# Performance work log

Hardware: AMD Instinct MI355X
Metric: run time of the kernel (lower is better)

## Reference

```python
import jax, jax.numpy as jnp
import numpy as np

T, D, H = 1024, 256, 256


def mish(x):
    return x * jnp.tanh(jax.nn.softplus(x))


def layer_norm(x, w, b, eps=1e-5):
    mu = x.mean(-1, keepdims=True)
    var = ((x - mu) ** 2).mean(-1, keepdims=True)
    return (x - mu) / jnp.sqrt(var + eps) * w + b


def setup_inputs() -> dict:
    key = jax.random.key(0)
    ks = jax.random.split(key, 12)
    def glorot(k, sh, fan_in):
        return (jax.random.normal(k, sh, jnp.float32) / np.sqrt(fan_in)).astype(jnp.float32)
    return {
        "x": jax.random.normal(ks[0], (T, D), jnp.float32),
        "s0": jnp.zeros((1, H, H), jnp.float32),
        "z0": jnp.zeros((1, H), jnp.float32),
        "start": jax.random.randint(ks[1], (T + 1,), 0, 2, jnp.int32),
        "done": jax.random.randint(ks[2], (T + 1,), 0, 2, jnp.int32),
        "Wk": glorot(ks[3], (H, D), D),
        "Wq": glorot(ks[4], (H, D), D),
        "Wv": glorot(ks[5], (H, D), D),
        "Wskip": glorot(ks[6], (H, D), D),
        "bskip": jnp.zeros((H,), jnp.float32),
        "W1": glorot(ks[7], (H, H), H),
        "b1": jnp.zeros((H,), jnp.float32),
        "W2": glorot(ks[8], (H, H), H),
        "b2": jnp.zeros((H,), jnp.float32),
        "W3": glorot(ks[9], (H, H), H),
        "b3": jnp.zeros((H,), jnp.float32),
        "ln_w": jnp.ones((H,), jnp.float32),
        "ln_b": jnp.zeros((H,), jnp.float32),
    }


def reference(x, s0, z0, start, done, Wk, Wq, Wv, Wskip, bskip, W1, b1, W2, b2, W3, b3, ln_w, ln_b):
    # feature maps (equinox Linear: y = W @ x, weight is (out,in))
    k = jax.nn.elu(x @ Wk.T)          # [T,H]
    q = jax.nn.elu(x @ Wq.T)          # [T,H]
    v = x @ Wv.T                      # [T,H]
    st = start.astype(x.dtype)[:, None]   # [T+1,1] reset-continuation flags
    dn = done.astype(x.dtype)[:, None]    # [T+1,1]
    # prepend carried state to the sequence, as in the original
    kv = jnp.concatenate([s0, jnp.einsum('ti,tj->tij', k, v)], axis=0)  # [T+1,H,H]
    kk = jnp.concatenate([z0, k], axis=0)                               # [T+1,H]
    def combine(a, b):
        s_a, z_a, _, _ = a
        kv_b, k_b, st_b, dn_b = b
        s = s_a * st_b[..., None] + kv_b * dn_b[..., None]
        z = z_a * st_b + k_b * dn_b
        return (s, z, st_b, dn_b)
    s, z, _, _ = jax.lax.associative_scan(combine, (kv, kk, st, dn))
    # drop the initial-state slot so time indices align with queries
    s_t, z_t = s[1:], z[1:]                          # [T,H,H], [T,H]
    numer = jnp.einsum('ti,tij->tj', q, s_t)         # [T,H]
    denom = jnp.einsum('ti,tj->t', z_t, q).clip(1e-5)  # faithful to source einsum
    out = numer / denom[:, None]
    h = mish(out @ W1.T + b1)
    h = mish(h @ W2.T + b2)
    h = h @ W3.T + b3
    return layer_norm(h + (x @ Wskip.T + bskip), ln_w, ln_b)
```

## Files before the change

### kernel.cpp

```cpp
#include <hip/hip_runtime.h>
#include <math.h>


typedef unsigned long long u64;
typedef unsigned short u16;
typedef __attribute__((ext_vector_type(8))) unsigned short us8;
typedef __attribute__((ext_vector_type(4))) unsigned short us4;
typedef __attribute__((ext_vector_type(8))) short s8;
typedef __attribute__((ext_vector_type(4))) float f4;

__device__ __forceinline__ float eluf(float v) { return v > 0.f ? v : expm1f(v); }
__device__ __forceinline__ float mishf(float v) {
  float sp = fmaxf(v, 0.f) + log1pf(expf(-fabsf(v)));
  return v * tanhf(sp);
}
__device__ __forceinline__ u16 f2bf(float f) {
  unsigned u = __float_as_uint(f);
  unsigned r = u + 0x7FFFu + ((u >> 16) & 1u);
  return (u16)(r >> 16);
}
__device__ __forceinline__ float bf2f(u16 h) { return __uint_as_float((unsigned)h << 16); }

__device__ __forceinline__ f4 mfma16(const u16* a, const u16* b, f4 c) {
  s8 av = *(const s8*)(const void*)a;
  s8 bv = *(const s8*)(const void*)b;
  return __builtin_amdgcn_mfma_f32_16x16x32_bf16(av, bv, c, 0, 0, 0);
}

__device__ __forceinline__ u64 expand32(u64 x) {
  x &= 0xFFFFFFFFull;
  x = (x | (x << 16)) & 0x0000FFFF0000FFFFull;
  x = (x | (x << 8))  & 0x00FF00FF00FF00FFull;
  x = (x | (x << 4))  & 0x0F0F0F0F0F0F0F0Full;
  x = (x | (x << 2))  & 0x3333333333333333ull;
  x = (x | (x << 1))  & 0x5555555555555555ull;
  return x | (x << 1);
}

__device__ __forceinline__ us8 cvt8v(float4 a, float4 b) {
  us8 v;
  v[0] = f2bf(a.x); v[1] = f2bf(a.y); v[2] = f2bf(a.z); v[3] = f2bf(a.w);
  v[4] = f2bf(b.x); v[5] = f2bf(b.y); v[6] = f2bf(b.z); v[7] = f2bf(b.w);
  return v;
}

__global__ __launch_bounds__(256) void qkvs_mfma(const float* __restrict__ x,
    const float* __restrict__ Wk, const float* __restrict__ Wq,
    const float* __restrict__ Wv, const float* __restrict__ Wsk,
    const float* __restrict__ bskip,
    const float* __restrict__ W1, const float* __restrict__ W2, const float* __restrict__ W3,
    u16* __restrict__ Kb, u16* __restrict__ Qb, u16* __restrict__ Vb,
    float* __restrict__ SKP, float* __restrict__ Kpart, u16* __restrict__ Wb) {
  __shared__ u16 Xs[64 * 40], Ws[64 * 40];
  const int tid = threadIdx.x, wave = tid >> 6, l = tid & 63;
  const int l15 = l & 15, quad = l >> 4;
  const int rt = blockIdx.x & 15, my = blockIdx.x >> 4;
  const int mat = my >> 2, nt = my & 3;
  const int n0 = nt * 64, mbase = rt * 64;
  const float* Wsrc = (mat == 0) ? Wk : (mat == 1) ? Wq : (mat == 2) ? Wv : Wsk;
  if (tid < 192) {
    int cidx = blockIdx.x * 768 + tid * 4;
    const float* Wm = (cidx < 65536) ? W1 : (cidx < 131072) ? W2 : W3;
    float4 v = *(const float4*)(Wm + (cidx & 65535));
    us4 o; o.x = f2bf(v.x); o.y = f2bf(v.y); o.z = f2bf(v.z); o.w = f2bf(v.w);
    *(us4*)&Wb[cidx] = o;
  }
  f4 acc[4];
#pragma unroll
  for (int s = 0; s < 4; s++) acc[s] = (f4){0.f, 0.f, 0.f, 0.f};
  const int srow = tid >> 2, sko = (tid & 3) * 8;
  const float* xp = &x[(mbase + srow) * 256 + sko];
  const float* wp = &Wsrc[(n0 + srow) * 256 + sko];
  float4 xa = *(const float4*)xp, xb = *(const float4*)(xp + 4);
  float4 wa = *(const float4*)wp, wc = *(const float4*)(wp + 4);
#pragma unroll 1
  for (int kt = 0; kt < 8; kt++) {
    *(us8*)&Xs[srow * 40 + sko] = cvt8v(xa, xb);
    *(us8*)&Ws[srow * 40 + sko] = cvt8v(wa, wc);
    if (kt < 7) {
      xa = *(const float4*)(xp + (kt + 1) * 32);
      xb = *(const float4*)(xp + (kt + 1) * 32 + 4);
      wa = *(const float4*)(wp + (kt + 1) * 32);
      wc = *(const float4*)(wp + (kt + 1) * 32 + 4);
    }
    __syncthreads();
    const u16* ap = &Xs[(wave * 16 + l15) * 40 + quad * 8];
#pragma unroll
    for (int s = 0; s < 4; s++)
      acc[s] = mfma16(ap, &Ws[(s * 16 + l15) * 40 + quad * 8], acc[s]);
    __syncthreads();
  }
  const int mw = mbase + wave * 16 + quad * 4;
  if (mat == 0) {
    float tmp[4][4];
#pragma unroll
    for (int s = 0; s < 4; s++)
#pragma unroll
      for (int r = 0; r < 4; r++) {
        float v = eluf(acc[s][r]);
        tmp[s][r] = v;
        Kb[(mw + r) * 256 + n0 + s * 16 + l15] = f2bf(v);
      }
#pragma unroll
    for (int r = 0; r < 4; r++) {
      float t = tmp[0][r] + tmp[1][r] + tmp[2][r] + tmp[3][r];
#pragma unroll
      for (int off = 1; off <= 8; off <<= 1) t += __shfl_xor(t, off);
      if (l15 == 0) Kpart[nt * 1024 + mw + r] = t;
    }
  } else if (mat == 1) {
#pragma unroll
    for (int s = 0; s < 4; s++)
#pragma unroll
      for (int r = 0; r < 4; r++)
        Qb[(mw + r) * 256 + n0 + s * 16 + l15] = f2bf(eluf(acc[s][r]));
  } else if (mat == 2) {
#pragma unroll
    for (int s = 0; s < 4; s++)
#pragma unroll
      for (int r = 0; r < 4; r++)
        Vb[(mw + r) * 256 + n0 + s * 16 + l15] = f2bf(acc[s][r]);
  } else {
#pragma unroll
    for (int s = 0; s < 4; s++) {
      int n = n0 + s * 16 + l15;
      float bv = bskip[n];
#pragma unroll
      for (int r = 0; r < 4; r++)
        SKP[(mw + r) * 256 + n] = acc[s][r] + bv;
    }
  }
}

__global__ __launch_bounds__(512) void attn_mlp(
    const u16* __restrict__ Kb, const u16* __restrict__ Qb, const u16* __restrict__ Vb,
    const float* __restrict__ Kpart, const float* __restrict__ SKP,
    const int* __restrict__ start, const int* __restrict__ done,
    const u16* __restrict__ Wb,
    const float* __restrict__ b1, const float* __restrict__ b2, const float* __restrict__ b3,
    const float* __restrict__ lnw, const float* __restrict__ lnb,
    float* __restrict__ outp) {
  __shared__ u64 GS[37];
  __shared__ u64 Mw[64];
  __shared__ u16 As[16 * 264];
  __shared__ float Op[8][256];
  __shared__ float dp[8];
  __shared__ float Hbuf[4 * 260];
  const int tid = threadIdx.x, wave = tid >> 6, l = tid & 63;
  const int l15 = l & 15, quad = l >> 4;
  const int m0 = blockIdx.x * 4;
  for (int job = wave; job < 37; job += 8) {
    int lv, w;
    if (job < 17)      { lv = 0; w = job; }
    else if (job < 25) { lv = 1; w = job - 17; }
    else if (job < 29) { lv = 2; w = job - 25; }
    else if (job < 31) { lv = 3; w = job - 29; }
    else               { lv = job - 27; w = 0; }
    int n = 1024 >> lv;
    int j = w * 64 + l;
    int ok = 0;
    if (j < n)
      ok = (j & 1) ? (done[((j + 1) << lv) - 1] != 0) : (start[((j + 2) << lv) - 1] != 0);
    u64 word = __ballot(ok != 0);
    if (l == 0) GS[(lv == 0) ? w : (lv == 1) ? 17 + w : (lv == 2) ? 25 + w
                   : (lv == 3) ? 29 + w : 27 + lv] = word;
  }
  __syncthreads();
  const int GOFF2[10] = {0, 17, 25, 29, 31, 32, 33, 34, 35, 36};
  if (wave < 4) {
    const int t = m0 + wave + 1;
    int rr10 = t;
#pragma unroll
    for (int q = 0; q < 10; q++) rr10 = (rr10 & 1) ? (rr10 >> 1) : (rr10 >> 1) - 1;
    u64 cur = (l == 0 && rr10 == 0) ? 1ull : 0ull;
#pragma unroll 1
    for (int lv = 9; lv >= 1; lv--) {
      int rr = t;
      for (int q = 0; q < lv; q++) rr = (rr & 1) ? (rr >> 1) : (rr >> 1) - 1;
      const int nw = (lv >= 4) ? 1 : (8 >> (lv - 1));
      u64 pw = __shfl(cur, l >> 1);
      u64 word;
      if (rr <= 0) word = (l == 0 && rr == 0) ? 1ull : 0ull;
      else {
        u64 e = 0;
        if (l < nw) e = expand32((l & 1) ? (pw >> 32) : pw) & GS[GOFF2[lv] + l];
        if (rr & 1) word = e;
        else {
          int gi = ((rr + 1) << lv) - 1;
          word = (start[gi] != 0) ? e : 0ull;
          if ((rr >> 6) == l) word |= (u64)(done[gi] != 0) << (rr & 63);
        }
        if (l >= nw) word = 0ull;
      }
      cur = word;
    }
    u64 pw = __shfl(cur, (l >> 1) & 7);
    u64 uw = 0;
    if (l <= 16) {
      u64 e = 0;
      if (l < 16) e = expand32((l & 1) ? (pw >> 32) : pw) & GS[l];
      if (t & 1) uw = e;
      else {
        uw = (start[t] != 0) ? e : 0ull;
        if ((t >> 6) == l) uw |= (u64)(done[t] != 0) << (t & 63);
      }
    }
    u64 nxt = __shfl(uw, (l + 1) & 63);
    u64 mw0 = (uw >> 1) | (nxt << 63);
    if (l < 16) Mw[wave * 16 + l] = mw0;
  }
  __syncthreads();
  const int r = wave & 3, h = wave >> 2;
  const int tp = m0 + r;
  float q[4], O[4] = {0.f, 0.f, 0.f, 0.f};
  {
    us4 qv = *(const us4*)&Qb[tp * 256 + l * 4];
    q[0] = bf2f(qv.x); q[1] = bf2f(qv.y); q[2] = bf2f(qv.z); q[3] = bf2f(qv.w);
  }
  float qs = q[0] + q[1] + q[2] + q[3];
#pragma unroll
  for (int off = 1; off <= 32; off <<= 1) qs += __shfl_xor(qs, off);
  float d = 0.f;
  for (int w = h * 8; w < h * 8 + 8; w++) {
    u64 bits = Mw[r * 16 + w];
    while (bits) {
      int b0 = __builtin_ctzll(bits); bits &= bits - 1;
      int j0 = w * 64 + b0;
      if (bits) {
        int b1x = __builtin_ctzll(bits); bits &= bits - 1;
        int j1 = w * 64 + b1x;
        us4 k0 = *(const us4*)&Kb[j0 * 256 + l * 4];
        us4 v0 = *(const us4*)&Vb[j0 * 256 + l * 4];
        us4 k1 = *(const us4*)&Kb[j1 * 256 + l * 4];
        us4 v1 = *(const us4*)&Vb[j1 * 256 + l * 4];
        float s0 = q[0] * bf2f(k0.x) + q[1] * bf2f(k0.y) + q[2] * bf2f(k0.z) + q[3] * bf2f(k0.w);
        float s1 = q[0] * bf2f(k1.x) + q[1] * bf2f(k1.y) + q[2] * bf2f(k1.z) + q[3] * bf2f(k1.w);
#pragma unroll
        for (int off = 1; off <= 32; off <<= 1) {
          s0 += __shfl_xor(s0, off);
          s1 += __shfl_xor(s1, off);
        }
        d += (Kpart[j0] + Kpart[1024 + j0] + Kpart[2048 + j0] + Kpart[3072 + j0]) +
             (Kpart[j1] + Kpart[1024 + j1] + Kpart[2048 + j1] + Kpart[3072 + j1]);
        O[0] += s0 * bf2f(v0.x) + s1 * bf2f(v1.x);
        O[1] += s0 * bf2f(v0.y) + s1 * bf2f(v1.y);
        O[2] += s0 * bf2f(v0.z) + s1 * bf2f(v1.z);
        O[3] += s0 * bf2f(v0.w) + s1 * bf2f(v1.w);
      } else {
        us4 k0 = *(const us4*)&Kb[j0 * 256 + l * 4];
        us4 v0 = *(const us4*)&Vb[j0 * 256 + l * 4];
        float s0 = q[0] * bf2f(k0.x) + q[1] * bf2f(k0.y) + q[2] * bf2f(k0.z) + q[3] * bf2f(k0.w);
#pragma unroll
        for (int off = 1; off <= 32; off <<= 1) s0 += __shfl_xor(s0, off);
        d += Kpart[j0] + Kpart[1024 + j0] + Kpart[2048 + j0] + Kpart[3072 + j0];
        O[0] += s0 * bf2f(v0.x); O[1] += s0 * bf2f(v0.y);
        O[2] += s0 * bf2f(v0.z); O[3] += s0 * bf2f(v0.w);
      }
    }
  }
#pragma unroll
  for (int i = 0; i < 4; i++) Op[wave][l * 4 + i] = O[i];
  if (l == 0) dp[wave] = d;
  __syncthreads();
  if (h == 0) {
    float dd = dp[r] + dp[r + 4];
    float inv = 1.f / fmaxf(qs * dd, 1e-5f);
    us4 o;
    o.x = f2bf((O[0] + Op[r + 4][l * 4 + 0]) * inv);
    o.y = f2bf((O[1] + Op[r + 4][l * 4 + 1]) * inv);
    o.z = f2bf((O[2] + Op[r + 4][l * 4 + 2]) * inv);
    o.w = f2bf((O[3] + Op[r + 4][l * 4 + 3]) * inv);
    *(us4*)&As[r * 264 + l * 4] = o;
  }
  __syncthreads();
#pragma unroll 1
  for (int layer = 0; layer < 3; layer++) {
    const u16* Wl = Wb + layer * 65536;
    const float* bias = (layer == 0) ? b1 : (layer == 1) ? b2 : b3;
    f4 acc[2];
#pragma unroll
    for (int c = 0; c < 2; c++) {
      const int nt = wave * 2 + c;
      acc[c] = (f4){0.f, 0.f, 0.f, 0.f};
#pragma unroll
      for (int kt = 0; kt < 8; kt++) {
        us8 bf = *(const us8*)&Wl[(nt * 16 + l15) * 256 + kt * 32 + quad * 8];
        acc[c] = mfma16(&As[l15 * 264 + kt * 32 + quad * 8], (const u16*)&bf, acc[c]);
      }
    }
    __syncthreads();
    if (quad == 0) {
#pragma unroll
      for (int c = 0; c < 2; c++) {
        const int n = (wave * 2 + c) * 16 + l15;
        float bv = bias[n];
        if (layer < 2) {
#pragma unroll
          for (int rr = 0; rr < 4; rr++)
            As[rr * 264 + n] = f2bf(mishf(acc[c][rr] + bv));
        } else {
#pragma unroll
          for (int rr = 0; rr < 4; rr++)
            Hbuf[rr * 260 + n] = acc[c][rr] + bv + SKP[(m0 + rr) * 256 + n];
        }
      }
    }
    __syncthreads();
  }
  if (wave < 4) {
    float hv[4];
#pragma unroll
    for (int i = 0; i < 4; i++) hv[i] = Hbuf[wave * 260 + l * 4 + i];
    float s1 = hv[0] + hv[1] + hv[2] + hv[3];
    float s2 = hv[0] * hv[0] + hv[1] * hv[1] + hv[2] * hv[2] + hv[3] * hv[3];
#pragma unroll
    for (int off = 1; off <= 32; off <<= 1) {
      s1 += __shfl_xor(s1, off);
      s2 += __shfl_xor(s2, off);
    }
    float mu = s1 * (1.f / 256.f);
    float var = s2 * (1.f / 256.f) - mu * mu;
    float rs = rsqrtf(fmaxf(var, 0.f) + 1e-5f);
    float4 wv = *(const float4*)&lnw[l * 4];
    float4 bv = *(const float4*)&lnb[l * 4];
    float4 o;
    o.x = (hv[0] - mu) * rs * wv.x + bv.x;
    o.y = (hv[1] - mu) * rs * wv.y + bv.y;
    o.z = (hv[2] - mu) * rs * wv.z + bv.z;
    o.w = (hv[3] - mu) * rs * wv.w + bv.w;
    *(float4*)&outp[(m0 + wave) * 256 + l * 4] = o;
  }
}

extern "C" void kernel_launch(void* const* d_in, const int* in_sizes, int n_in,
                              void* d_out, int out_size, void* d_ws, size_t ws_size,
                              hipStream_t stream) {
  (void)in_sizes; (void)n_in; (void)out_size; (void)ws_size;
  const float* x   = (const float*)d_in[0];
  const int* start = (const int*)d_in[3];
  const int* done  = (const int*)d_in[4];
  const float* Wk  = (const float*)d_in[5];
  const float* Wq  = (const float*)d_in[6];
  const float* Wv  = (const float*)d_in[7];
  const float* Wsk = (const float*)d_in[8];
  const float* bsk = (const float*)d_in[9];
  const float* W1  = (const float*)d_in[10];
  const float* b1  = (const float*)d_in[11];
  const float* W2  = (const float*)d_in[12];
  const float* b2  = (const float*)d_in[13];
  const float* W3  = (const float*)d_in[14];
  const float* b3  = (const float*)d_in[15];
  const float* lnw = (const float*)d_in[16];
  const float* lnb = (const float*)d_in[17];
  float* out = (float*)d_out;

  char* w = (char*)d_ws;
  u16* Kb      = (u16*)w;
  u16* Qb      = (u16*)(w + 524288);
  u16* Vb      = (u16*)(w + 1048576);
  float* SKP   = (float*)(w + 1572864);
  float* Kpart = (float*)(w + 2621440);
  u16* Wb      = (u16*)(w + 2637824);

  qkvs_mfma<<<256, 256, 0, stream>>>(x, Wk, Wq, Wv, Wsk, bsk, W1, W2, W3,
                                     Kb, Qb, Vb, SKP, Kpart, Wb);
  attn_mlp<<<256, 512, 0, stream>>>(Kb, Qb, Vb, Kpart, SKP, start, done, Wb,
                                    b1, b2, b3, lnw, lnb, out);
}
```

Measured before the change: 129.5 us.

## Fuse projection and attention kernels into one cooperative launch with grid sync

Merges the QKV/skip projection kernel and the attention+MLP kernel into a single cooperative kernel separated by a grid-wide barrier. The projection GEMM now reads fp32 operands directly into registers and drops the LDS staging and block barriers, with each of 8 waves computing two 16x16 tiles. The start/done mask ballots and scan-mask computation run before the grid sync so they overlap the projection work. This aims to remove one kernel launch gap and shared-memory round trips, at the cost of a grid-wide sync and the occupancy requirement that all 256 blocks be co-resident.

```diff
diff --git a/kernel.cpp b/kernel.cpp
--- a/kernel.cpp
+++ b/kernel.cpp
@@ -1,6 +1,9 @@
 #include <hip/hip_runtime.h>
+#include <hip/hip_cooperative_groups.h>
 #include <math.h>
 
+
+namespace cg = cooperative_groups;
 
 typedef unsigned long long u64;
 typedef unsigned short u16;
@@ -44,126 +47,122 @@
   return v;
 }
 
-__global__ __launch_bounds__(256) void qkvs_mfma(const float* __restrict__ x,
-    const float* __restrict__ Wk, const float* __restrict__ Wq,
-    const float* __restrict__ Wv, const float* __restrict__ Wsk,
-    const float* __restrict__ bskip,
-    const float* __restrict__ W1, const float* __restrict__ W2, const float* __restrict__ W3,
+__global__ __launch_bounds__(512) void fused(
+    const float* __restrict__ x, const float* __restrict__ Wk,
+    const float* __restrict__ Wq, const float* __restrict__ Wv,
+    const float* __restrict__ Wsk, const float* __restrict__ bskip,
+    const int* __restrict__ start, const int* __restrict__ done,
+    const float* __restrict__ W1, const float* __restrict__ W2,
+    const float* __restrict__ W3, const float* __restrict__ b1,
+    const float* __restrict__ b2, const float* __restrict__ b3,
+    const float* __restrict__ lnw, const float* __restrict__ lnb,
     u16* __restrict__ Kb, u16* __restrict__ Qb, u16* __restrict__ Vb,
-    float* __restrict__ SKP, float* __restrict__ Kpart, u16* __restrict__ Wb) {
-  __shared__ u16 Xs[64 * 40], Ws[64 * 40];
-  const int tid = threadIdx.x, wave = tid >> 6, l = tid & 63;
-  const int l15 = l & 15, quad = l >> 4;
-  const int rt = blockIdx.x & 15, my = blockIdx.x >> 4;
-  const int mat = my >> 2, nt = my & 3;
-  const int n0 = nt * 64, mbase = rt * 64;
-  const float* Wsrc = (mat == 0) ? Wk : (mat == 1) ? Wq : (mat == 2) ? Wv : Wsk;
-  if (tid < 192) {
-    int cidx = blockIdx.x * 768 + tid * 4;
-    const float* Wm = (cidx < 65536) ? W1 : (cidx < 131072) ? W2 : W3;
-    float4 v = *(const float4*)(Wm + (cidx & 65535));
-    us4 o; o.x = f2bf(v.x); o.y = f2bf(v.y); o.z = f2bf(v.z); o.w = f2bf(v.w);
-    *(us4*)&Wb[cidx] = o;
-  }
-  f4 acc[4];
-#pragma unroll
-  for (int s = 0; s < 4; s++) acc[s] = (f4){0.f, 0.f, 0.f, 0.f};
-  const int srow = tid >> 2, sko = (tid & 3) * 8;
-  const float* xp = &x[(mbase + srow) * 256 + sko];
-  const float* wp = &Wsrc[(n0 + srow) * 256 + sko];
-  float4 xa = *(const float4*)xp, xb = *(const float4*)(xp + 4);
-  float4 wa = *(const float4*)wp, wc = *(const float4*)(wp + 4);
-#pragma unroll 1
-  for (int kt = 0; kt < 8; kt++) {
-    *(us8*)&Xs[srow * 40 + sko] = cvt8v(xa, xb);
-    *(us8*)&Ws[srow * 40 + sko] = cvt8v(wa, wc);
-    if (kt < 7) {
-      xa = *(const float4*)(xp + (kt + 1) * 32);
-      xb = *(const float4*)(xp + (kt + 1) * 32 + 4);
-      wa = *(const float4*)(wp + (kt + 1) * 32);
-      wc = *(const float4*)(wp + (kt + 1) * 32 + 4);
-    }
-    __syncthreads();
-    const u16* ap = &Xs[(wave * 16 + l15) * 40 + quad * 8];
-#pragma unroll
-    for (int s = 0; s < 4; s++)
-      acc[s] = mfma16(ap, &Ws[(s * 16 + l15) * 40 + quad * 8], acc[s]);
-    __syncthreads();
-  }
-  const int mw = mbase + wave * 16 + quad * 4;
-  if (mat == 0) {
-    float tmp[4][4];
-#pragma unroll
-    for (int s = 0; s < 4; s++)
-#pragma unroll
-      for (int r = 0; r < 4; r++) {
-        float v = eluf(acc[s][r]);
-        tmp[s][r] = v;
-        Kb[(mw + r) * 256 + n0 + s * 16 + l15] = f2bf(v);
-      }
-#pragma unroll
-    for (int r = 0; r < 4; r++) {
-      float t = tmp[0][r] + tmp[1][r] + tmp[2][r] + tmp[3][r];
-#pragma unroll
-      for (int off = 1; off <= 8; off <<= 1) t += __shfl_xor(t, off);
-      if (l15 == 0) Kpart[nt * 1024 + mw + r] = t;
-    }
-  } else if (mat == 1) {
-#pragma unroll
-    for (int s = 0; s < 4; s++)
-#pragma unroll
-      for (int r = 0; r < 4; r++)
-        Qb[(mw + r) * 256 + n0 + s * 16 + l15] = f2bf(eluf(acc[s][r]));
-  } else if (mat == 2) {
-#pragma unroll
-    for (int s = 0; s < 4; s++)
-#pragma unroll
-      for (int r = 0; r < 4; r++)
-        Vb[(mw + r) * 256 + n0 + s * 16 + l15] = f2bf(acc[s][r]);
-  } else {
-#pragma unroll
-    for (int s = 0; s < 4; s++) {
-      int n = n0 + s * 16 + l15;
-      float bv = bskip[n];
-#pragma unroll
-      for (int r = 0; r < 4; r++)
-        SKP[(mw + r) * 256 + n] = acc[s][r] + bv;
-    }
-  }
-}
-
-__global__ __launch_bounds__(512) void attn_mlp(
-    const u16* __restrict__ Kb, const u16* __restrict__ Qb, const u16* __restrict__ Vb,
-    const float* __restrict__ Kpart, const float* __restrict__ SKP,
-    const int* __restrict__ start, const int* __restrict__ done,
-    const u16* __restrict__ Wb,
-    const float* __restrict__ b1, const float* __restrict__ b2, const float* __restrict__ b3,
-    const float* __restrict__ lnw, const float* __restrict__ lnb,
+    float* __restrict__ SKP, float* __restrict__ Kpart, u16* __restrict__ Wb,
     float* __restrict__ outp) {
   __shared__ u64 GS[37];
   __shared__ u64 Mw[64];
+  __shared__ float scrK[128];
   __shared__ u16 As[16 * 264];
   __shared__ float Op[8][256];
   __shared__ float dp[8];
   __shared__ float Hbuf[4 * 260];
   const int tid = threadIdx.x, wave = tid >> 6, l = tid & 63;
   const int l15 = l & 15, quad = l >> 4;
-  const int m0 = blockIdx.x * 4;
-  for (int job = wave; job < 37; job += 8) {
-    int lv, w;
-    if (job < 17)      { lv = 0; w = job; }
-    else if (job < 25) { lv = 1; w = job - 17; }
-    else if (job < 29) { lv = 2; w = job - 25; }
-    else if (job < 31) { lv = 3; w = job - 29; }
-    else               { lv = job - 27; w = 0; }
-    int n = 1024 >> lv;
-    int j = w * 64 + l;
-    int ok = 0;
-    if (j < n)
-      ok = (j & 1) ? (done[((j + 1) << lv) - 1] != 0) : (start[((j + 2) << lv) - 1] != 0);
-    u64 word = __ballot(ok != 0);
-    if (l == 0) GS[(lv == 0) ? w : (lv == 1) ? 17 + w : (lv == 2) ? 25 + w
-                   : (lv == 3) ? 29 + w : 27 + lv] = word;
+  const int b = blockIdx.x;
+  const int m0 = b * 4;
+
+  if (tid < 192) {
+    int cidx = b * 768 + tid * 4;
+    const float* Wm = (cidx < 65536) ? W1 : (cidx < 131072) ? W2 : W3;
+    float4 v = *(const float4*)(Wm + (cidx & 65535));
+    us4 o; o.x = f2bf(v.x); o.y = f2bf(v.y); o.z = f2bf(v.z); o.w = f2bf(v.w);
+    *(us4*)&Wb[cidx] = o;
+  }
+
+  const int rt = b & 15, my = b >> 4, mat = my >> 2, nt = my & 3;
+  const int n0 = nt * 64, mbase = rt * 64;
+  const float* Wsrc = (mat == 0) ? Wk : (mat == 1) ? Wq : (mat == 2) ? Wv : Wsk;
+  const int st = wave & 3, sh = (wave >> 2) * 2;
+  const int arow = mbase + st * 16 + l15;
+  f4 acc[2];
+  acc[0] = (f4){0.f, 0.f, 0.f, 0.f};
+  acc[1] = (f4){0.f, 0.f, 0.f, 0.f};
+  {
+    const float* apb = x + (size_t)arow * 256 + quad * 8;
+    const float* bp0 = Wsrc + (size_t)(n0 + sh * 16 + l15) * 256 + quad * 8;
+    const float* bp1 = bp0 + 16 * 256;
+#pragma unroll 1
+    for (int kt = 0; kt < 8; kt++) {
+      const int ko = kt * 32;
+      float4 a0 = *(const float4*)(apb + ko), a1 = *(const float4*)(apb + ko + 4);
+      float4 c0 = *(const float4*)(bp0 + ko), c1 = *(const float4*)(bp0 + ko + 4);
+      float4 d0 = *(const float4*)(bp1 + ko), d1 = *(const float4*)(bp1 + ko + 4);
+      us8 af = cvt8v(a0, a1);
+      us8 bf0 = cvt8v(c0, c1);
+      us8 bf1 = cvt8v(d0, d1);
+      acc[0] = mfma16((const u16*)&af, (const u16*)&bf0, acc[0]);
+      acc[1] = mfma16((const u16*)&af, (const u16*)&bf1, acc[1]);
+    }
+  }
+  const int mw = mbase + st * 16 + quad * 4;
+  if (mat == 0) {
+    float tw[4];
+#pragma unroll
+    for (int r = 0; r < 4; r++) {
+      float v0 = eluf(acc[0][r]), v1 = eluf(acc[1][r]);
+      Kb[(mw + r) * 256 + n0 + sh * 16 + l15] = f2bf(v0);
+      Kb[(mw + r) * 256 + n0 + (sh + 1) * 16 + l15] = f2bf(v1);
+      tw[r] = v0 + v1;
+    }
+#pragma unroll
+    for (int r = 0; r < 4; r++) {
+      float t = tw[r];
+#pragma unroll
+      for (int off = 1; off <= 8; off <<= 1) t += __shfl_xor(t, off);
+      if (l15 == 0) scrK[st * 32 + (wave >> 2) * 16 + quad * 4 + r] = t;
+    }
+  } else if (mat == 1) {
+#pragma unroll
+    for (int c = 0; c < 2; c++)
+#pragma unroll
+      for (int r = 0; r < 4; r++)
+        Qb[(mw + r) * 256 + n0 + (sh + c) * 16 + l15] = f2bf(eluf(acc[c][r]));
+  } else if (mat == 2) {
+#pragma unroll
+    for (int c = 0; c < 2; c++)
+#pragma unroll
+      for (int r = 0; r < 4; r++)
+        Vb[(mw + r) * 256 + n0 + (sh + c) * 16 + l15] = f2bf(acc[c][r]);
+  } else {
+#pragma unroll
+    for (int c = 0; c < 2; c++) {
+      int n = n0 + (sh + c) * 16 + l15;
+      float bv = bskip[n];
+#pragma unroll
+      for (int r = 0; r < 4; r++)
+        SKP[(mw + r) * 256 + n] = acc[c][r] + bv;
+    }
+  }
+  __syncthreads();
+  if (mat == 0 && wave < 4 && l < 16)
+    Kpart[nt * 1024 + mbase + wave * 16 + l] = scrK[wave * 32 + l] + scrK[wave * 32 + 16 + l];
+  if (wave >= 4) {
+    for (int job = wave - 4; job < 37; job += 4) {
+      int lv, w;
+      if (job < 17)      { lv = 0; w = job; }
+      else if (job < 25) { lv = 1; w = job - 17; }
+      else if (job < 29) { lv = 2; w = job - 25; }
+      else if (job < 31) { lv = 3; w = job - 29; }
+      else               { lv = job - 27; w = 0; }
+      int n = 1024 >> lv;
+      int j = w * 64 + l;
+      int ok = 0;
+      if (j < n)
+        ok = (j & 1) ? (done[((j + 1) << lv) - 1] != 0) : (start[((j + 2) << lv) - 1] != 0);
+      u64 word = __ballot(ok != 0);
+      if (l == 0) GS[(lv == 0) ? w : (lv == 1) ? 17 + w : (lv == 2) ? 25 + w
+                     : (lv == 3) ? 29 + w : 27 + lv] = word;
+    }
   }
   __syncthreads();
   const int GOFF2[10] = {0, 17, 25, 29, 31, 32, 33, 34, 35, 36};
@@ -210,6 +209,9 @@
     if (l < 16) Mw[wave * 16 + l] = mw0;
   }
   __syncthreads();
+
+  cg::this_grid().sync();
+
   const int r = wave & 3, h = wave >> 2;
   const int tp = m0 + r;
   float q[4], O[4] = {0.f, 0.f, 0.f, 0.f};
@@ -277,15 +279,15 @@
   for (int layer = 0; layer < 3; layer++) {
     const u16* Wl = Wb + layer * 65536;
     const float* bias = (layer == 0) ? b1 : (layer == 1) ? b2 : b3;
-    f4 acc[2];
+    f4 acc2[2];
 #pragma unroll
     for (int c = 0; c < 2; c++) {
-      const int nt = wave * 2 + c;
-      acc[c] = (f4){0.f, 0.f, 0.f, 0.f};
+      const int ntc = wave * 2 + c;
+      acc2[c] = (f4){0.f, 0.f, 0.f, 0.f};
 #pragma unroll
       for (int kt = 0; kt < 8; kt++) {
-        us8 bf = *(const us8*)&Wl[(nt * 16 + l15) * 256 + kt * 32 + quad * 8];
-        acc[c] = mfma16(&As[l15 * 264 + kt * 32 + quad * 8], (const u16*)&bf, acc[c]);
+        us8 bf = *(const us8*)&Wl[(ntc * 16 + l15) * 256 + kt * 32 + quad * 8];
+        acc2[c] = mfma16(&As[l15 * 264 + kt * 32 + quad * 8], (const u16*)&bf, acc2[c]);
       }
     }
     __syncthreads();
@@ -297,11 +299,11 @@
         if (layer < 2) {
 #pragma unroll
           for (int rr = 0; rr < 4; rr++)
-            As[rr * 264 + n] = f2bf(mishf(acc[c][rr] + bv));
+            As[rr * 264 + n] = f2bf(mishf(acc2[c][rr] + bv));
         } else {
 #pragma unroll
           for (int rr = 0; rr < 4; rr++)
-            Hbuf[rr * 260 + n] = acc[c][rr] + bv + SKP[(m0 + rr) * 256 + n];
+            Hbuf[rr * 260 + n] = acc2[c][rr] + bv + SKP[(m0 + rr) * 256 + n];
         }
       }
     }
@@ -362,8 +364,13 @@
   float* Kpart = (float*)(w + 2621440);
   u16* Wb      = (u16*)(w + 2637824);
 
-  qkvs_mfma<<<256, 256, 0, stream>>>(x, Wk, Wq, Wv, Wsk, bsk, W1, W2, W3,
-                                     Kb, Qb, Vb, SKP, Kpart, Wb);
-  attn_mlp<<<256, 512, 0, stream>>>(Kb, Qb, Vb, Kpart, SKP, start, done, Wb,
-                                    b1, b2, b3, lnw, lnb, out);
-}
+  void* args[] = {
+    (void*)&x, (void*)&Wk, (void*)&Wq, (void*)&Wv, (void*)&Wsk, (void*)&bsk,
+    (void*)&start, (void*)&done, (void*)&W1, (void*)&W2, (void*)&W3,
+    (void*)&b1, (void*)&b2, (void*)&b3, (void*)&lnw, (void*)&lnb,
+    (void*)&Kb, (void*)&Qb, (void*)&Vb, (void*)&SKP, (void*)&Kpart,
+    (void*)&Wb, (void*)&out
+  };
+  hipLaunchCooperativeKernel((const void*)fused, dim3(256), dim3(512),
+                             args, 0, stream);
+}
```

After: 189.7 us. 1.46x slower.

## Double-buffer projection GEMM with 512 threads and halve rows per attention block

Applied to the files above, without the earlier changes.

The projection kernel now runs 512 threads: half of them stage x tiles and half stage weight tiles into double-buffered LDS, which drops one barrier per k-step. Each wave now computes two MFMA tiles instead of four, and the K row sums are reduced through shared scratch. The attention/MLP kernel processes 2 query rows per block instead of 4, doubling the grid to 512 blocks and splitting each row's history across 4 waves instead of 2. The aim is more parallelism and less serial scan work per block, at the cost of reading the MLP weights twice as often and leaving half of each MFMA tile idle.

```diff
diff --git a/kernel.cpp b/kernel.cpp
--- a/kernel.cpp
+++ b/kernel.cpp
@@ -44,14 +44,15 @@
   return v;
 }
 
-__global__ __launch_bounds__(256) void qkvs_mfma(const float* __restrict__ x,
+__global__ __launch_bounds__(512) void qkvs_mfma(const float* __restrict__ x,
     const float* __restrict__ Wk, const float* __restrict__ Wq,
     const float* __restrict__ Wv, const float* __restrict__ Wsk,
     const float* __restrict__ bskip,
     const float* __restrict__ W1, const float* __restrict__ W2, const float* __restrict__ W3,
     u16* __restrict__ Kb, u16* __restrict__ Qb, u16* __restrict__ Vb,
     float* __restrict__ SKP, float* __restrict__ Kpart, u16* __restrict__ Wb) {
-  __shared__ u16 Xs[64 * 40], Ws[64 * 40];
+  __shared__ u16 Xs[2][64 * 40], Ws[2][64 * 40];
+  __shared__ float scrK[128];
   const int tid = threadIdx.x, wave = tid >> 6, l = tid & 63;
   const int l15 = l & 15, quad = l >> 4;
   const int rt = blockIdx.x & 15, my = blockIdx.x >> 4;
@@ -65,69 +66,65 @@
     us4 o; o.x = f2bf(v.x); o.y = f2bf(v.y); o.z = f2bf(v.z); o.w = f2bf(v.w);
     *(us4*)&Wb[cidx] = o;
   }
-  f4 acc[4];
-#pragma unroll
-  for (int s = 0; s < 4; s++) acc[s] = (f4){0.f, 0.f, 0.f, 0.f};
-  const int srow = tid >> 2, sko = (tid & 3) * 8;
-  const float* xp = &x[(mbase + srow) * 256 + sko];
-  const float* wp = &Wsrc[(n0 + srow) * 256 + sko];
-  float4 xa = *(const float4*)xp, xb = *(const float4*)(xp + 4);
-  float4 wa = *(const float4*)wp, wc = *(const float4*)(wp + 4);
+  const int sidx = tid & 255, srow = sidx >> 2, sko = (sidx & 3) * 8;
+  const int isB = tid >> 8;
+  const float* src = (isB ? Wsrc + (size_t)(n0 + srow) * 256
+                          : x + (size_t)(mbase + srow) * 256) + sko;
+  u16* dstb = (isB ? &Ws[0][0] : &Xs[0][0]) + srow * 40 + sko;
+  const int st = wave & 3, sh = (wave >> 2) * 2;
+  f4 acc0 = (f4){0.f, 0.f, 0.f, 0.f}, acc1 = (f4){0.f, 0.f, 0.f, 0.f};
+  float4 pa = *(const float4*)src, pb = *(const float4*)(src + 4);
 #pragma unroll 1
   for (int kt = 0; kt < 8; kt++) {
-    *(us8*)&Xs[srow * 40 + sko] = cvt8v(xa, xb);
-    *(us8*)&Ws[srow * 40 + sko] = cvt8v(wa, wc);
+    const int p = kt & 1;
+    *(us8*)(dstb + p * 2560) = cvt8v(pa, pb);
     if (kt < 7) {
-      xa = *(const float4*)(xp + (kt + 1) * 32);
-      xb = *(const float4*)(xp + (kt + 1) * 32 + 4);
-      wa = *(const float4*)(wp + (kt + 1) * 32);
-      wc = *(const float4*)(wp + (kt + 1) * 32 + 4);
+      pa = *(const float4*)(src + (kt + 1) * 32);
+      pb = *(const float4*)(src + (kt + 1) * 32 + 4);
     }
     __syncthreads();
-    const u16* ap = &Xs[(wave * 16 + l15) * 40 + quad * 8];
-#pragma unroll
-    for (int s = 0; s < 4; s++)
-      acc[s] = mfma16(ap, &Ws[(s * 16 + l15) * 40 + quad * 8], acc[s]);
+    const u16* ap = &Xs[p][(st * 16 + l15) * 40 + quad * 8];
+    acc0 = mfma16(ap, &Ws[p][(sh * 16 + l15) * 40 + quad * 8], acc0);
+    acc1 = mfma16(ap, &Ws[p][((sh + 1) * 16 + l15) * 40 + quad * 8], acc1);
+  }
+  const int mw = mbase + st * 16 + quad * 4;
+  if (mat == 0) {
+    float tw[4];
+#pragma unroll
+    for (int r = 0; r < 4; r++) {
+      float v0 = eluf(acc0[r]), v1 = eluf(acc1[r]);
+      Kb[(mw + r) * 256 + n0 + sh * 16 + l15] = f2bf(v0);
+      Kb[(mw + r) * 256 + n0 + (sh + 1) * 16 + l15] = f2bf(v1);
+      tw[r] = v0 + v1;
+    }
+#pragma unroll
+    for (int r = 0; r < 4; r++) {
+      float t = tw[r];
+#pragma unroll
+      for (int off = 1; off <= 8; off <<= 1) t += __shfl_xor(t, off);
+      if (l15 == 0) scrK[st * 32 + (wave >> 2) * 16 + quad * 4 + r] = t;
+    }
     __syncthreads();
-  }
-  const int mw = mbase + wave * 16 + quad * 4;
-  if (mat == 0) {
-    float tmp[4][4];
-#pragma unroll
-    for (int s = 0; s < 4; s++)
-#pragma unroll
-      for (int r = 0; r < 4; r++) {
-        float v = eluf(acc[s][r]);
-        tmp[s][r] = v;
-        Kb[(mw + r) * 256 + n0 + s * 16 + l15] = f2bf(v);
-      }
-#pragma unroll
-    for (int r = 0; r < 4; r++) {
-      float t = tmp[0][r] + tmp[1][r] + tmp[2][r] + tmp[3][r];
-#pragma unroll
-      for (int off = 1; off <= 8; off <<= 1) t += __shfl_xor(t, off);
-      if (l15 == 0) Kpart[nt * 1024 + mw + r] = t;
-    }
+    if (wave < 4 && l < 16)
+      Kpart[nt * 1024 + mbase + wave * 16 + l] = scrK[wave * 32 + l] + scrK[wave * 32 + 16 + l];
   } else if (mat == 1) {
 #pragma unroll
-    for (int s = 0; s < 4; s++)
-#pragma unroll
-      for (int r = 0; r < 4; r++)
-        Qb[(mw + r) * 256 + n0 + s * 16 + l15] = f2bf(eluf(acc[s][r]));
+    for (int r = 0; r < 4; r++) {
+      Qb[(mw + r) * 256 + n0 + sh * 16 + l15] = f2bf(eluf(acc0[r]));
+      Qb[(mw + r) * 256 + n0 + (sh + 1) * 16 + l15] = f2bf(eluf(acc1[r]));
+    }
   } else if (mat == 2) {
 #pragma unroll
-    for (int s = 0; s < 4; s++)
-#pragma unroll
-      for (int r = 0; r < 4; r++)
-        Vb[(mw + r) * 256 + n0 + s * 16 + l15] = f2bf(acc[s][r]);
+    for (int r = 0; r < 4; r++) {
+      Vb[(mw + r) * 256 + n0 + sh * 16 + l15] = f2bf(acc0[r]);
+      Vb[(mw + r) * 256 + n0 + (sh + 1) * 16 + l15] = f2bf(acc1[r]);
+    }
   } else {
-#pragma unroll
-    for (int s = 0; s < 4; s++) {
-      int n = n0 + s * 16 + l15;
-      float bv = bskip[n];
-#pragma unroll
-      for (int r = 0; r < 4; r++)
-        SKP[(mw + r) * 256 + n] = acc[s][r] + bv;
+    float bv0 = bskip[n0 + sh * 16 + l15], bv1 = bskip[n0 + (sh + 1) * 16 + l15];
+#pragma unroll
+    for (int r = 0; r < 4; r++) {
+      SKP[(mw + r) * 256 + n0 + sh * 16 + l15] = acc0[r] + bv0;
+      SKP[(mw + r) * 256 + n0 + (sh + 1) * 16 + l15] = acc1[r] + bv1;
     }
   }
 }
@@ -141,14 +138,14 @@
     const float* __restrict__ lnw, const float* __restrict__ lnb,
     float* __restrict__ outp) {
   __shared__ u64 GS[37];
-  __shared__ u64 Mw[64];
+  __shared__ u64 Mw[32];
   __shared__ u16 As[16 * 264];
   __shared__ float Op[8][256];
   __shared__ float dp[8];
-  __shared__ float Hbuf[4 * 260];
+  __shared__ float Hbuf[2 * 260];
   const int tid = threadIdx.x, wave = tid >> 6, l = tid & 63;
   const int l15 = l & 15, quad = l >> 4;
-  const int m0 = blockIdx.x * 4;
+  const int m0 = blockIdx.x * 2;
   for (int job = wave; job < 37; job += 8) {
     int lv, w;
     if (job < 17)      { lv = 0; w = job; }
@@ -167,7 +164,7 @@
   }
   __syncthreads();
   const int GOFF2[10] = {0, 17, 25, 29, 31, 32, 33, 34, 35, 36};
-  if (wave < 4) {
+  if (wave < 2) {
     const int t = m0 + wave + 1;
     int rr10 = t;
 #pragma unroll
@@ -210,7 +207,7 @@
     if (l < 16) Mw[wave * 16 + l] = mw0;
   }
   __syncthreads();
-  const int r = wave & 3, h = wave >> 2;
+  const int r = wave & 1, h = wave >> 1;
   const int tp = m0 + r;
   float q[4], O[4] = {0.f, 0.f, 0.f, 0.f};
   {
@@ -221,7 +218,7 @@
 #pragma unroll
   for (int off = 1; off <= 32; off <<= 1) qs += __shfl_xor(qs, off);
   float d = 0.f;
-  for (int w = h * 8; w < h * 8 + 8; w++) {
+  for (int w = h * 4; w < h * 4 + 4; w++) {
     u64 bits = Mw[r * 16 + w];
     while (bits) {
       int b0 = __builtin_ctzll(bits); bits &= bits - 1;
@@ -263,13 +260,13 @@
   if (l == 0) dp[wave] = d;
   __syncthreads();
   if (h == 0) {
-    float dd = dp[r] + dp[r + 4];
+    float dd = dp[r] + dp[r + 2] + dp[r + 4] + dp[r + 6];
     float inv = 1.f / fmaxf(qs * dd, 1e-5f);
     us4 o;
-    o.x = f2bf((O[0] + Op[r + 4][l * 4 + 0]) * inv);
-    o.y = f2bf((O[1] + Op[r + 4][l * 4 + 1]) * inv);
-    o.z = f2bf((O[2] + Op[r + 4][l * 4 + 2]) * inv);
-    o.w = f2bf((O[3] + Op[r + 4][l * 4 + 3]) * inv);
+    o.x = f2bf((O[0] + Op[r + 2][l * 4 + 0] + Op[r + 4][l * 4 + 0] + Op[r + 6][l * 4 + 0]) * inv);
+    o.y = f2bf((O[1] + Op[r + 2][l * 4 + 1] + Op[r + 4][l * 4 + 1] + Op[r + 6][l * 4 + 1]) * inv);
+    o.z = f2bf((O[2] + Op[r + 2][l * 4 + 2] + Op[r + 4][l * 4 + 2] + Op[r + 6][l * 4 + 2]) * inv);
+    o.w = f2bf((O[3] + Op[r + 2][l * 4 + 3] + Op[r + 4][l * 4 + 3] + Op[r + 6][l * 4 + 3]) * inv);
     *(us4*)&As[r * 264 + l * 4] = o;
   }
   __syncthreads();
@@ -277,15 +274,15 @@
   for (int layer = 0; layer < 3; layer++) {
     const u16* Wl = Wb + layer * 65536;
     const float* bias = (layer == 0) ? b1 : (layer == 1) ? b2 : b3;
-    f4 acc[2];
+    f4 acc2[2];
 #pragma unroll
     for (int c = 0; c < 2; c++) {
-      const int nt = wave * 2 + c;
-      acc[c] = (f4){0.f, 0.f, 0.f, 0.f};
+      const int ntc = wave * 2 + c;
+      acc2[c] = (f4){0.f, 0.f, 0.f, 0.f};
 #pragma unroll
       for (int kt = 0; kt < 8; kt++) {
-        us8 bf = *(const us8*)&Wl[(nt * 16 + l15) * 256 + kt * 32 + quad * 8];
-        acc[c] = mfma16(&As[l15 * 264 + kt * 32 + quad * 8], (const u16*)&bf, acc[c]);
+        us8 bf = *(const us8*)&Wl[(ntc * 16 + l15) * 256 + kt * 32 + quad * 8];
+        acc2[c] = mfma16(&As[l15 * 264 + kt * 32 + quad * 8], (const u16*)&bf, acc2[c]);
       }
     }
     __syncthreads();
@@ -296,18 +293,18 @@
         float bv = bias[n];
         if (layer < 2) {
 #pragma unroll
-          for (int rr = 0; rr < 4; rr++)
-            As[rr * 264 + n] = f2bf(mishf(acc[c][rr] + bv));
+          for (int rr = 0; rr < 2; rr++)
+            As[rr * 264 + n] = f2bf(mishf(acc2[c][rr] + bv));
         } else {
 #pragma unroll
-          for (int rr = 0; rr < 4; rr++)
-            Hbuf[rr * 260 + n] = acc[c][rr] + bv + SKP[(m0 + rr) * 256 + n];
+          for (int rr = 0; rr < 2; rr++)
+            Hbuf[rr * 260 + n] = acc2[c][rr] + bv + SKP[(m0 + rr) * 256 + n];
         }
       }
     }
     __syncthreads();
   }
-  if (wave < 4) {
+  if (wave < 2) {
     float hv[4];
 #pragma unroll
     for (int i = 0; i < 4; i++) hv[i] = Hbuf[wave * 260 + l * 4 + i];
@@ -362,8 +359,8 @@
   float* Kpart = (float*)(w + 2621440);
   u16* Wb      = (u16*)(w + 2637824);
 
-  qkvs_mfma<<<256, 256, 0, stream>>>(x, Wk, Wq, Wv, Wsk, bsk, W1, W2, W3,
+  qkvs_mfma<<<256, 512, 0, stream>>>(x, Wk, Wq, Wv, Wsk, bsk, W1, W2, W3,
                                      Kb, Qb, Vb, SKP, Kpart, Wb);
-  attn_mlp<<<256, 512, 0, stream>>>(Kb, Qb, Vb, Kpart, SKP, start, done, Wb,
+  attn_mlp<<<512, 512, 0, stream>>>(Kb, Qb, Vb, Kpart, SKP, start, done, Wb,
                                     b1, b2, b3, lnw, lnb, out);
 }
```

After: 134.0 us. +3.5%, slower.
